# Kernel optimization log

Measured on AMD Instinct MI355X. Metric: run time of the kernel, lower is better.

Reference implementation:

```python
import jax, jax.numpy as jnp
import numpy as np

B, N, DIM = 2, 2048, 1024
H, DH = 8, 64
NUM_BUCKETS, MAX_DISTANCE = 32, 128


def _rel_bucket(rel_pos, num_buckets=NUM_BUCKETS, max_distance=MAX_DISTANCE):
    # torch: n = max(-rel_pos, 0); causal (non-bidirectional) bucketing
    n = jnp.maximum(-rel_pos, 0)
    max_exact = num_buckets // 2
    is_small = n < max_exact
    n_safe = jnp.maximum(n, 1)  # avoid log(0); masked out by is_small anyway
    val_if_large = max_exact + (
        jnp.log(n_safe.astype(jnp.float32) / max_exact)
        / np.log(max_distance / max_exact)
        * (num_buckets - max_exact)
    ).astype(jnp.int32)
    val_if_large = jnp.minimum(val_if_large, num_buckets - 1)
    return jnp.where(is_small, n, val_if_large)


def setup_inputs() -> dict:
    key = jax.random.key(0)
    ks = jax.random.split(key, 10)
    inner = H * DH
    return {
        "x": jax.random.normal(ks[0], (B, N, DIM), jnp.float32),
        "mem_kv": jax.random.normal(ks[1], (B, H * N, 2, DH), jnp.float32),
        "mem_mask": jnp.ones((B, H * N), dtype=bool),
        "Wq": jax.random.normal(ks[2], (DIM, inner), jnp.float32) * (DIM ** -0.5),
        "Wkv": jax.random.normal(ks[3], (DIM, 2 * DH), jnp.float32) * (DIM ** -0.5),
        "Wout": jax.random.normal(ks[4], (inner, DIM), jnp.float32) * (inner ** -0.5),
        "bout": jnp.zeros((DIM,), jnp.float32),
        "rel_emb": jax.random.normal(ks[5], (NUM_BUCKETS, H), jnp.float32),
        "gate": jax.random.normal(ks[6], (H, 1, 1), jnp.float32),
        "null_k": jax.random.normal(ks[7], (DH,), jnp.float32),
        "null_v": jax.random.normal(ks[8], (DH,), jnp.float32),
    }


def reference(x, mem_kv, mem_mask, Wq, Wkv, Wout, bout, rel_emb, gate, null_k, null_v):
    b, n, _ = x.shape
    scale = DH ** -0.5
    q = (x @ Wq).reshape(b, n, H, DH).transpose(0, 2, 1, 3)  # b h n d
    k, v = jnp.split(x @ Wkv, 2, axis=-1)  # each b n d (multi-query: head-shared)

    # local causal attention with T5 relative position bias
    sim = jnp.einsum('bhid,bjd->bhij', q, k) * scale
    pos = jnp.arange(n)
    rel = pos[None, :] - pos[:, None]  # k_pos - q_pos
    bias = rel_emb[_rel_bucket(rel)]  # [n, n, h]
    sim = sim + jnp.transpose(bias, (2, 0, 1))[None] * (DH ** 0.5)
    mask_value = -jnp.finfo(sim.dtype).max
    causal = jnp.triu(jnp.ones((n, n), dtype=bool), 1)
    sim = jnp.where(causal, mask_value, sim)
    attn = jax.nn.softmax(sim, axis=-1)
    local_values = jnp.einsum('bhij,bjd->bhid', attn, v)

    # retrieval (kNN memory) attention branch
    mem = mem_kv.reshape(b, H, n, 2, DH)
    mem_k, mem_v = mem[..., 0, :], mem[..., 1, :]  # b h n d
    null_k_b = jnp.broadcast_to(null_k, (b, H, 1, DH))
    null_v_b = jnp.broadcast_to(null_v, (b, H, 1, DH))
    mem_k = jnp.concatenate([null_k_b, mem_k], axis=2)  # b h (n+1) d
    mem_v = jnp.concatenate([null_v_b, mem_v], axis=2)
    mm = mem_mask.reshape(b, H, 1, n)
    mm = jnp.pad(mm, ((0, 0), (0, 0), (0, 0), (1, 0)), constant_values=True)
    sim_mem = jnp.einsum('bhid,bhjd->bhij', q, mem_k) * scale
    sim_mem = jnp.where(mm, sim_mem, mask_value)
    attn_mem = jax.nn.softmax(sim_mem, axis=-1)
    mem_values = jnp.einsum('bhij,bhjd->bhid', attn_mem, mem_v)

    g = jax.nn.sigmoid(gate)  # [h,1,1] broadcasts over b h n d
    out = local_values * g + mem_values * (1.0 - g)
    out = out.transpose(0, 2, 1, 3).reshape(b, n, H * DH)
    return out @ Wout + bout
```

## Files before the change

kernel.cpp:

```cpp
#include <hip/hip_runtime.h>
#include <hip/hip_fp16.h>

typedef _Float16 f16x8 __attribute__((ext_vector_type(8)));
typedef _Float16 f16x4 __attribute__((ext_vector_type(4)));
typedef __fp16 fp16x2_t __attribute__((ext_vector_type(2)));
typedef float f32x4 __attribute__((ext_vector_type(4)));
typedef float f32x16 __attribute__((ext_vector_type(16)));
typedef unsigned int uint;
typedef uint u32x4 __attribute__((ext_vector_type(4)));

#define NB 2
#define NN 2048
#define NDIM 1024
#define NH 8
#define NDH 64
#define NINNER 512
#define NJM 2080

#define QSCALE 0.18033688011112042f
#define BSCALE 11.541560327111707f


__global__ void conv_x_kernel(const float* __restrict__ x, _Float16* __restrict__ xh) {
  int i = (blockIdx.x * blockDim.x + threadIdx.x) * 4;
  float4 f = *(const float4*)(x + i);
  xh[i + 0] = (_Float16)f.x;
  xh[i + 1] = (_Float16)f.y;
  xh[i + 2] = (_Float16)f.z;
  xh[i + 3] = (_Float16)f.w;
}

__global__ void conv_wt_kernel(const float* __restrict__ Wq, const float* __restrict__ Wkv,
                               _Float16* __restrict__ wt) {
  int idx = blockIdx.x * blockDim.x + threadIdx.x;
  int c = idx >> 10, k = idx & 1023;
  float v = (c < NINNER) ? Wq[(size_t)k * NINNER + c] : Wkv[(size_t)k * 128 + (c - NINNER)];
  wt[idx] = (_Float16)v;
}

__global__ void conv_woutT_kernel(const float* __restrict__ Wout, _Float16* __restrict__ woutT) {
  int idx = blockIdx.x * blockDim.x + threadIdx.x;
  int c = idx >> 9, k = idx & 511;
  woutT[idx] = (_Float16)Wout[(size_t)k * NDIM + c];
}

__global__ __launch_bounds__(256)
void conv_mem_kernel(const float* __restrict__ mem_kv,
                     _Float16* __restrict__ memk, _Float16* __restrict__ memvt) {
  __shared__ _Float16 tv[32][76];
  int jc = blockIdx.x, bh = blockIdx.y;
  int t = threadIdx.x;
  int jl = t >> 3, c = (t & 7) * 8;
  int j0 = jc * 32;
  const float* src = mem_kv + (((size_t)bh * NN) + (j0 + jl)) * 128;
  float4 k0 = *(const float4*)(src + c);
  float4 k1 = *(const float4*)(src + c + 4);
  float4 v0 = *(const float4*)(src + 64 + c);
  float4 v1 = *(const float4*)(src + 64 + c + 4);
  f16x8 kk;
  kk[0]=(_Float16)k0.x; kk[1]=(_Float16)k0.y; kk[2]=(_Float16)k0.z; kk[3]=(_Float16)k0.w;
  kk[4]=(_Float16)k1.x; kk[5]=(_Float16)k1.y; kk[6]=(_Float16)k1.z; kk[7]=(_Float16)k1.w;
  *(f16x8*)(memk + ((size_t)bh * NJM + j0 + jl) * NDH + c) = kk;
  tv[jl][c+0]=(_Float16)v0.x; tv[jl][c+1]=(_Float16)v0.y;
  tv[jl][c+2]=(_Float16)v0.z; tv[jl][c+3]=(_Float16)v0.w;
  tv[jl][c+4]=(_Float16)v1.x; tv[jl][c+5]=(_Float16)v1.y;
  tv[jl][c+6]=(_Float16)v1.z; tv[jl][c+7]=(_Float16)v1.w;
  __syncthreads();
  int d = t >> 2, j8 = (t & 3) * 8;
  f16x8 vv;
#pragma unroll
  for (int u = 0; u < 8; ++u) vv[u] = tv[j8 + u][d];
  *(f16x8*)(memvt + (((size_t)bh * NDH) + d) * NJM + j0 + j8) = vv;
}

__global__ void conv_tail_kernel(const float* __restrict__ null_k, const float* __restrict__ null_v,
                                 _Float16* __restrict__ memk, _Float16* __restrict__ memvt) {
  int t = blockIdx.x * blockDim.x + threadIdx.x;
  int d = t & 63, bh = t >> 6;
  memk[((size_t)bh * NJM + NN) * NDH + d] = (_Float16)null_k[d];
  memvt[(((size_t)bh * NDH) + d) * NJM + NN] = (_Float16)null_v[d];
  for (int r = NN + 1; r < NJM; ++r) {
    memk[((size_t)bh * NJM + r) * NDH + d] = (_Float16)0.f;
    memvt[(((size_t)bh * NDH) + d) * NJM + r] = (_Float16)0.f;
  }
}

__global__ void bias_kernel(const float* __restrict__ rel_emb, float* __restrict__ bias_tab) {
  int idx = blockIdx.x * blockDim.x + threadIdx.x;
  int h = idx >> 11, d = idx & (NN - 1);
  int bucket;
  if (d < 16) bucket = d;
  else {
    float t = logf((float)d * (1.0f / 16.0f)) / 2.0794415416798357f * 16.0f;
    bucket = 16 + (int)t;
    if (bucket > 31) bucket = 31;
  }
  bias_tab[idx] = rel_emb[bucket * NH + h] * BSCALE;
}

__global__ __launch_bounds__(256)
void proj_kernel(const _Float16* __restrict__ xh, const _Float16* __restrict__ wt,
                 _Float16* __restrict__ qh, _Float16* __restrict__ kh, _Float16* __restrict__ vtL) {
  int lane = threadIdx.x & 63, w = threadIdx.x >> 6;
  int wm = w >> 1, wn = w & 1;
  int m0 = blockIdx.x * 64 + wm * 32;
  int n0 = blockIdx.y * 64 + wn * 32;
  int lane_c = lane & 15, lane_g = lane >> 4;
  f32x4 acc[2][2] = {};
  for (int kk = 0; kk < NDIM; kk += 32) {
    f16x8 a[2], bb[2];
#pragma unroll
    for (int s = 0; s < 2; ++s) {
      a[s]  = *(const f16x8*)(xh + (size_t)(m0 + s * 16 + lane_c) * NDIM + kk + lane_g * 8);
      bb[s] = *(const f16x8*)(wt + (size_t)(n0 + s * 16 + lane_c) * NDIM + kk + lane_g * 8);
    }
#pragma unroll
    for (int ms = 0; ms < 2; ++ms)
#pragma unroll
      for (int ns = 0; ns < 2; ++ns)
        acc[ms][ns] = __builtin_amdgcn_mfma_f32_16x16x32_f16(a[ms], bb[ns], acc[ms][ns], 0, 0, 0);
  }
#pragma unroll
  for (int ms = 0; ms < 2; ++ms)
#pragma unroll
    for (int ns = 0; ns < 2; ++ns) {
      int c = n0 + ns * 16 + lane_c;
      int mb = m0 + ms * 16 + lane_g * 4;
      int b = mb >> 11, n = mb & (NN - 1);
      if (c < NINNER) {
        int h = c >> 6, d = c & 63;
#pragma unroll
        for (int r = 0; r < 4; ++r)
          qh[(((size_t)(b * NH + h)) * NN + n + r) * NDH + d] = (_Float16)(acc[ms][ns][r] * QSCALE);
      } else if (c < NINNER + NDH) {
#pragma unroll
        for (int r = 0; r < 4; ++r)
          kh[((size_t)(b * NN + n + r)) * NDH + (c - NINNER)] = (_Float16)acc[ms][ns][r];
      } else {
        f16x4 pv;
#pragma unroll
        for (int r = 0; r < 4; ++r) pv[r] = (_Float16)acc[ms][ns][r];
        *(f16x4*)(vtL + ((size_t)(b * NDH + (c - NINNER - NDH))) * NN + n) = pv;
      }
    }
}


__device__ __forceinline__ uint pkrtz(float a, float b) {
  fp16x2_t t = __builtin_amdgcn_cvt_pkrtz(a, b);
  return __builtin_bit_cast(uint, t);
}

struct K4 { f16x8 k[4]; };

__device__ __forceinline__ K4 load_k4(const _Float16* kp) {
  K4 r;
  r.k[0] = *(const f16x8*)(kp);
  r.k[1] = *(const f16x8*)(kp + 16);
  r.k[2] = *(const f16x8*)(kp + 32);
  r.k[3] = *(const f16x8*)(kp + 48);
  return r;
}

template<int MODE, int LDV>
__device__ __forceinline__ void compute_tile(
    const K4& kc, const _Float16* vp, const f16x8* qf,
    int dd_base, int li, bool hib,
    const float* s_bias, float bias31,
    f32x16& o0, f32x16& o1, float& m, float& l)
{
  f16x8 v00 = *(const f16x8*)(vp);
  f16x8 v01 = *(const f16x8*)(vp + 16);
  f16x8 v10 = *(const f16x8*)(vp + (size_t)32 * LDV);
  f16x8 v11 = *(const f16x8*)(vp + (size_t)32 * LDV + 16);
  f32x16 sA = {}, sB = {};
  sA = __builtin_amdgcn_mfma_f32_32x32x16_f16(kc.k[0], qf[0], sA, 0, 0, 0);
  sB = __builtin_amdgcn_mfma_f32_32x32x16_f16(kc.k[1], qf[1], sB, 0, 0, 0);
  sA = __builtin_amdgcn_mfma_f32_32x32x16_f16(kc.k[2], qf[2], sA, 0, 0, 0);
  sB = __builtin_amdgcn_mfma_f32_32x32x16_f16(kc.k[3], qf[3], sB, 0, 0, 0);
  int hi4 = hib ? 4 : 0;
  float p[16];
  float pmax = -1e30f;
#pragma unroll
  for (int r = 0; r < 16; ++r) {
    int jp = (r & 3) + 8 * (r >> 2) + hi4;
    float v = sA[r] + sB[r];
    if (MODE == 0) { v += bias31; }
    else if (MODE == 1) { int d = dd_base + li - jp; v += (d >= 113) ? bias31 : s_bias[d]; }
    else if (MODE == 2) { int d = li - jp; float bb = s_bias[d < 0 ? 0 : d];
                          v = (jp > li) ? -1e30f : (v + bb); }
    else if (MODE == 4) { v = (jp >= 1) ? -1e30f : v; }
    p[r] = v;
    pmax = fmaxf(pmax, v);
  }
  pmax = fmaxf(pmax, __shfl_xor(pmax, 32));
  if (!__all(pmax <= m + 8.0f)) {
    float mn = fmaxf(m, pmax);
    float f = exp2f(m - mn);
#pragma unroll
    for (int r = 0; r < 16; ++r) { o0[r] *= f; o1[r] *= f; }
    l *= f; m = mn;
  }
  float rs = 0.f;
  uint u[8];
#pragma unroll
  for (int q = 0; q < 8; ++q) {
    float pa = exp2f(p[2 * q] - m), pb = exp2f(p[2 * q + 1] - m);
    rs += pa + pb;
    u[q] = pkrtz(pa, pb);
  }
  rs += __shfl_xor(rs, 32);
  l += rs;
  uint x0 = __shfl_xor(u[0], 32), x1 = __shfl_xor(u[1], 32);
  uint x2 = __shfl_xor(u[2], 32), x3 = __shfl_xor(u[3], 32);
  uint x4 = __shfl_xor(u[4], 32), x5 = __shfl_xor(u[5], 32);
  uint x6 = __shfl_xor(u[6], 32), x7 = __shfl_xor(u[7], 32);
  u32x4 b0u = { hib ? x2 : u[0], hib ? x3 : u[1], hib ? u[2] : x0, hib ? u[3] : x1 };
  u32x4 b1u = { hib ? x6 : u[4], hib ? x7 : u[5], hib ? u[6] : x4, hib ? u[7] : x5 };
  f16x8 b0 = __builtin_bit_cast(f16x8, b0u);
  f16x8 b1 = __builtin_bit_cast(f16x8, b1u);
  o0 = __builtin_amdgcn_mfma_f32_32x32x16_f16(v00, b0, o0, 0, 0, 0);
  o0 = __builtin_amdgcn_mfma_f32_32x32x16_f16(v01, b1, o0, 0, 0, 0);
  o1 = __builtin_amdgcn_mfma_f32_32x32x16_f16(v10, b0, o1, 0, 0, 0);
  o1 = __builtin_amdgcn_mfma_f32_32x32x16_f16(v11, b1, o1, 0, 0, 0);
}

__global__ __launch_bounds__(128, 2)
void attn_kernel(const _Float16* __restrict__ qh, const _Float16* __restrict__ kh,
                 const _Float16* __restrict__ vtL, const _Float16* __restrict__ memk,
                 const _Float16* __restrict__ memvt, const float* __restrict__ bias_tab,
                 const float* __restrict__ gate, _Float16* __restrict__ comb) {
  __shared__ float s_bias[128];
  __shared__ float s_o[2][16][64];
  int bid = blockIdx.x;
  int h = bid & 7, b = (bid >> 3) & 1, qt = 63 - (bid >> 4);
  int tid = threadIdx.x;
  int w = tid >> 6, lane = tid & 63;
  int li = lane & 31;
  bool hib = lane >= 32;
  int i0 = qt * 32;
  int bh = b * NH + h;

  const _Float16* qp = qh + (((size_t)bh * NN) + i0 + li) * NDH + (hib ? 8 : 0);
  f16x8 qf[4];
#pragma unroll
  for (int ks = 0; ks < 4; ++ks) qf[ks] = *(const f16x8*)(qp + ks * 16);

  float gv = gate[h];
  gv = 1.0f / (1.0f + __expf(-gv));
  f32x16 o0 = {}, o1 = {};
  float m = -INFINITY, l = 0.f;

  if (w == 0) {
    s_bias[lane] = bias_tab[h * NN + lane];
    s_bias[lane + 64] = bias_tab[h * NN + lane + 64];
    float bias31 = bias_tab[h * NN + 127];
    const _Float16* kB = kh + (size_t)b * NN * NDH + (size_t)li * NDH + (hib ? 8 : 0);
    const _Float16* vB = vtL + (size_t)b * NDH * NN + (size_t)li * NN + (hib ? 8 : 0);
    int nfar = (i0 - 160) < 0 ? 0 : (((i0 - 160) >> 5) + 1);
    K4 kc = load_k4(kB);
    int t = 0;
    for (; t < nfar; ++t) {
      K4 kn = load_k4(kB + (size_t)(t + 1) * 32 * NDH);
      compute_tile<0, NN>(kc, vB + t * 32, qf, 0, li, hib, s_bias, bias31, o0, o1, m, l);
      kc = kn;
    }
    for (; t < qt; ++t) {
      K4 kn = load_k4(kB + (size_t)(t + 1) * 32 * NDH);
      compute_tile<1, NN>(kc, vB + t * 32, qf, i0 - t * 32, li, hib, s_bias, bias31, o0, o1, m, l);
      kc = kn;
    }
    compute_tile<2, NN>(kc, vB + qt * 32, qf, 0, li, hib, s_bias, bias31, o0, o1, m, l);
  } else {
    const _Float16* kB = memk + (size_t)bh * NJM * NDH + (size_t)li * NDH + (hib ? 8 : 0);
    const _Float16* vB = memvt + (size_t)bh * NDH * NJM + (size_t)li * NJM + (hib ? 8 : 0);
    K4 kc = load_k4(kB);
    for (int t = 0; t < 64; ++t) {
      K4 kn = load_k4(kB + (size_t)(t + 1) * 32 * NDH);
      compute_tile<3, NJM>(kc, vB + t * 32, qf, 0, li, hib, nullptr, 0.f, o0, o1, m, l);
      kc = kn;
    }
    compute_tile<4, NJM>(kc, vB + 64 * 32, qf, 0, li, hib, nullptr, 0.f, o0, o1, m, l);
    float invl = (1.0f - gv) / l;
#pragma unroll
    for (int r = 0; r < 16; ++r) {
      s_o[0][r][lane] = o0[r] * invl;
      s_o[1][r][lane] = o1[r] * invl;
    }
  }
  __syncthreads();
  if (w == 0) {
    float invl = gv / l;
    int i = i0 + li;
    _Float16* cp = comb + ((size_t)(b * NN + i)) * NINNER + h * NDH + (hib ? 4 : 0);
#pragma unroll
    for (int db = 0; db < 2; ++db) {
#pragma unroll
      for (int g = 0; g < 4; ++g) {
        f16x4 st;
#pragma unroll
        for (int r = 0; r < 4; ++r) {
          float ov = (db ? o1[g * 4 + r] : o0[g * 4 + r]) * invl + s_o[db][g * 4 + r][lane];
          st[r] = (_Float16)ov;
        }
        *(f16x4*)(cp + db * 32 + g * 8) = st;
      }
    }
  }
}

__global__ __launch_bounds__(256)
void out_kernel(const _Float16* __restrict__ comb, const _Float16* __restrict__ woutT,
                const float* __restrict__ bout, float* __restrict__ out) {
  int lane = threadIdx.x & 63, w = threadIdx.x >> 6;
  int wm = w >> 1, wn = w & 1;
  int m0 = blockIdx.x * 64 + wm * 32;
  int n0 = blockIdx.y * 64 + wn * 32;
  int lane_c = lane & 15, lane_g = lane >> 4;
  f32x4 acc[2][2] = {};
  for (int kk = 0; kk < NINNER; kk += 32) {
    f16x8 a[2], bb[2];
#pragma unroll
    for (int s = 0; s < 2; ++s) {
      a[s]  = *(const f16x8*)(comb + (size_t)(m0 + s * 16 + lane_c) * NINNER + kk + lane_g * 8);
      bb[s] = *(const f16x8*)(woutT + (size_t)(n0 + s * 16 + lane_c) * NINNER + kk + lane_g * 8);
    }
#pragma unroll
    for (int ms = 0; ms < 2; ++ms)
#pragma unroll
      for (int ns = 0; ns < 2; ++ns)
        acc[ms][ns] = __builtin_amdgcn_mfma_f32_16x16x32_f16(a[ms], bb[ns], acc[ms][ns], 0, 0, 0);
  }
#pragma unroll
  for (int ms = 0; ms < 2; ++ms)
#pragma unroll
    for (int ns = 0; ns < 2; ++ns)
#pragma unroll
      for (int r = 0; r < 4; ++r) {
        int mrow = m0 + ms * 16 + lane_g * 4 + r;
        int c = n0 + ns * 16 + lane_c;
        out[(size_t)mrow * NDIM + c] = acc[ms][ns][r] + bout[c];
      }
}

extern "C" void kernel_launch(void* const* d_in, const int* in_sizes, int n_in,
                              void* d_out, int out_size, void* d_ws, size_t ws_size,
                              hipStream_t stream) {
  const float* x      = (const float*)d_in[0];
  const float* mem_kv = (const float*)d_in[1];
  const float* Wq     = (const float*)d_in[3];
  const float* Wkv    = (const float*)d_in[4];
  const float* Wout   = (const float*)d_in[5];
  const float* bout   = (const float*)d_in[6];
  const float* rel_emb = (const float*)d_in[7];
  const float* gate   = (const float*)d_in[8];
  const float* null_k = (const float*)d_in[9];
  const float* null_v = (const float*)d_in[10];
  float* out = (float*)d_out;
  char* ws = (char*)d_ws;

  _Float16* xh    = (_Float16*)(ws + 0);
  _Float16* wt    = (_Float16*)(ws + 8388608);
  _Float16* woutT = (_Float16*)(ws + 9699328);
  _Float16* qh    = (_Float16*)(ws + 10747904);
  _Float16* kh    = (_Float16*)(ws + 14942208);
  _Float16* vtL   = (_Float16*)(ws + 15466496);
  _Float16* memk  = (_Float16*)(ws + 15990784);
  _Float16* memvt = (_Float16*)(ws + 20250624);
  _Float16* comb  = (_Float16*)(ws + 24510464);
  float* bias_tab = (float*)(ws + 28704768);

  conv_x_kernel<<<4096, 256, 0, stream>>>(x, xh);
  conv_wt_kernel<<<2560, 256, 0, stream>>>(Wq, Wkv, wt);
  conv_woutT_kernel<<<2048, 256, 0, stream>>>(Wout, woutT);
  conv_mem_kernel<<<dim3(64, 16), 256, 0, stream>>>(mem_kv, memk, memvt);
  conv_tail_kernel<<<4, 256, 0, stream>>>(null_k, null_v, memk, memvt);
  bias_kernel<<<64, 256, 0, stream>>>(rel_emb, bias_tab);
  proj_kernel<<<dim3(64, 10), 256, 0, stream>>>(xh, wt, qh, kh, vtL);
  attn_kernel<<<1024, 128, 0, stream>>>(qh, kh, vtL, memk, memvt, bias_tab, gate, comb);
  out_kernel<<<dim3(64, 16), 256, 0, stream>>>(comb, woutT, bout, out);
}
```

Before: 188.9 us.

## Split attention KV range across waves with merge, fuse prep kernels, add setprio

The attention kernel now uses 4 waves instead of 2. Two waves split the local causal tiles by even/odd index and two split the memory tiles in halves, and partial softmax states are merged through shared memory. The small conversion, bias and tail kernels are fused into one prep kernel to cut launch overhead. The K/V row stride is padded to KROWS so prefetch past the end stays in bounds. The change also adds s_setprio around MFMAs and tree reductions for max/sum. Risks are more shared memory and sync per block, plus extra merge arithmetic.

```diff
diff --git a/kernel.cpp b/kernel.cpp
--- a/kernel.cpp
+++ b/kernel.cpp
@@ -16,32 +16,55 @@
 #define NDH 64
 #define NINNER 512
 #define NJM 2080
+#define KROWS 2112
 
 #define QSCALE 0.18033688011112042f
 #define BSCALE 11.541560327111707f
 
-
-__global__ void conv_x_kernel(const float* __restrict__ x, _Float16* __restrict__ xh) {
-  int i = (blockIdx.x * blockDim.x + threadIdx.x) * 4;
-  float4 f = *(const float4*)(x + i);
-  xh[i + 0] = (_Float16)f.x;
-  xh[i + 1] = (_Float16)f.y;
-  xh[i + 2] = (_Float16)f.z;
-  xh[i + 3] = (_Float16)f.w;
-}
-
-__global__ void conv_wt_kernel(const float* __restrict__ Wq, const float* __restrict__ Wkv,
-                               _Float16* __restrict__ wt) {
-  int idx = blockIdx.x * blockDim.x + threadIdx.x;
-  int c = idx >> 10, k = idx & 1023;
-  float v = (c < NINNER) ? Wq[(size_t)k * NINNER + c] : Wkv[(size_t)k * 128 + (c - NINNER)];
-  wt[idx] = (_Float16)v;
-}
-
-__global__ void conv_woutT_kernel(const float* __restrict__ Wout, _Float16* __restrict__ woutT) {
-  int idx = blockIdx.x * blockDim.x + threadIdx.x;
-  int c = idx >> 9, k = idx & 511;
-  woutT[idx] = (_Float16)Wout[(size_t)k * NDIM + c];
+__global__ __launch_bounds__(256)
+void prep_kernel(const float* __restrict__ x, _Float16* __restrict__ xh,
+                 const float* __restrict__ Wq, const float* __restrict__ Wkv,
+                 _Float16* __restrict__ wt,
+                 const float* __restrict__ Wout, _Float16* __restrict__ woutT,
+                 const float* __restrict__ null_k, const float* __restrict__ null_v,
+                 _Float16* __restrict__ memk, _Float16* __restrict__ memvt,
+                 const float* __restrict__ rel_emb, float* __restrict__ bias_tab) {
+  int bx = blockIdx.x, t = threadIdx.x;
+  if (bx < 4096) {
+    int i = (bx * 256 + t) * 4;
+    float4 f = *(const float4*)(x + i);
+    f16x4 o; o[0]=(_Float16)f.x; o[1]=(_Float16)f.y; o[2]=(_Float16)f.z; o[3]=(_Float16)f.w;
+    *(f16x4*)(xh + i) = o;
+  } else if (bx < 6656) {
+    int idx = (bx - 4096) * 256 + t;
+    int c = idx >> 10, k = idx & 1023;
+    float v = (c < NINNER) ? Wq[(size_t)k * NINNER + c] : Wkv[(size_t)k * 128 + (c - NINNER)];
+    wt[idx] = (_Float16)v;
+  } else if (bx < 8704) {
+    int idx = (bx - 6656) * 256 + t;
+    int c = idx >> 9, k = idx & 511;
+    woutT[idx] = (_Float16)Wout[(size_t)k * NDIM + c];
+  } else if (bx < 8768) {
+    int idx = (bx - 8704) * 256 + t;
+    int h = idx >> 11, d = idx & (NN - 1);
+    int bucket;
+    if (d < 16) bucket = d;
+    else {
+      float tt = logf((float)d * (1.0f / 16.0f)) / 2.0794415416798357f * 16.0f;
+      bucket = 16 + (int)tt;
+      if (bucket > 31) bucket = 31;
+    }
+    bias_tab[idx] = rel_emb[bucket * NH + h] * BSCALE;
+  } else {
+    int idx = (bx - 8768) * 256 + t;
+    int d = idx & 63, bh = idx >> 6;
+    memk[((size_t)bh * NJM + NN) * NDH + d] = (_Float16)null_k[d];
+    memvt[(((size_t)bh * NDH) + d) * NJM + NN] = (_Float16)null_v[d];
+    for (int r = NN + 1; r < NJM; ++r) {
+      memk[((size_t)bh * NJM + r) * NDH + d] = (_Float16)0.f;
+      memvt[(((size_t)bh * NDH) + d) * NJM + r] = (_Float16)0.f;
+    }
+  }
 }
 
 __global__ __launch_bounds__(256)
@@ -73,31 +96,6 @@
   *(f16x8*)(memvt + (((size_t)bh * NDH) + d) * NJM + j0 + j8) = vv;
 }
 
-__global__ void conv_tail_kernel(const float* __restrict__ null_k, const float* __restrict__ null_v,
-                                 _Float16* __restrict__ memk, _Float16* __restrict__ memvt) {
-  int t = blockIdx.x * blockDim.x + threadIdx.x;
-  int d = t & 63, bh = t >> 6;
-  memk[((size_t)bh * NJM + NN) * NDH + d] = (_Float16)null_k[d];
-  memvt[(((size_t)bh * NDH) + d) * NJM + NN] = (_Float16)null_v[d];
-  for (int r = NN + 1; r < NJM; ++r) {
-    memk[((size_t)bh * NJM + r) * NDH + d] = (_Float16)0.f;
-    memvt[(((size_t)bh * NDH) + d) * NJM + r] = (_Float16)0.f;
-  }
-}
-
-__global__ void bias_kernel(const float* __restrict__ rel_emb, float* __restrict__ bias_tab) {
-  int idx = blockIdx.x * blockDim.x + threadIdx.x;
-  int h = idx >> 11, d = idx & (NN - 1);
-  int bucket;
-  if (d < 16) bucket = d;
-  else {
-    float t = logf((float)d * (1.0f / 16.0f)) / 2.0794415416798357f * 16.0f;
-    bucket = 16 + (int)t;
-    if (bucket > 31) bucket = 31;
-  }
-  bias_tab[idx] = rel_emb[bucket * NH + h] * BSCALE;
-}
-
 __global__ __launch_bounds__(256)
 void proj_kernel(const _Float16* __restrict__ xh, const _Float16* __restrict__ wt,
                  _Float16* __restrict__ qh, _Float16* __restrict__ kh, _Float16* __restrict__ vtL) {
@@ -135,12 +133,12 @@
       } else if (c < NINNER + NDH) {
 #pragma unroll
         for (int r = 0; r < 4; ++r)
-          kh[((size_t)(b * NN + n + r)) * NDH + (c - NINNER)] = (_Float16)acc[ms][ns][r];
+          kh[((size_t)(b * KROWS + n + r)) * NDH + (c - NINNER)] = (_Float16)acc[ms][ns][r];
       } else {
         f16x4 pv;
 #pragma unroll
         for (int r = 0; r < 4; ++r) pv[r] = (_Float16)acc[ms][ns][r];
-        *(f16x4*)(vtL + ((size_t)(b * NDH + (c - NINNER - NDH))) * NN + n) = pv;
+        *(f16x4*)(vtL + ((size_t)(b * NDH + (c - NINNER - NDH))) * KROWS + n) = pv;
       }
     }
 }
@@ -174,13 +172,14 @@
   f16x8 v10 = *(const f16x8*)(vp + (size_t)32 * LDV);
   f16x8 v11 = *(const f16x8*)(vp + (size_t)32 * LDV + 16);
   f32x16 sA = {}, sB = {};
+  __builtin_amdgcn_s_setprio(1);
   sA = __builtin_amdgcn_mfma_f32_32x32x16_f16(kc.k[0], qf[0], sA, 0, 0, 0);
   sB = __builtin_amdgcn_mfma_f32_32x32x16_f16(kc.k[1], qf[1], sB, 0, 0, 0);
   sA = __builtin_amdgcn_mfma_f32_32x32x16_f16(kc.k[2], qf[2], sA, 0, 0, 0);
   sB = __builtin_amdgcn_mfma_f32_32x32x16_f16(kc.k[3], qf[3], sB, 0, 0, 0);
+  __builtin_amdgcn_s_setprio(0);
   int hi4 = hib ? 4 : 0;
   float p[16];
-  float pmax = -1e30f;
 #pragma unroll
   for (int r = 0; r < 16; ++r) {
     int jp = (r & 3) + 8 * (r >> 2) + hi4;
@@ -191,8 +190,13 @@
                           v = (jp > li) ? -1e30f : (v + bb); }
     else if (MODE == 4) { v = (jp >= 1) ? -1e30f : v; }
     p[r] = v;
-    pmax = fmaxf(pmax, v);
-  }
+  }
+  float t8[8], t4[4];
+#pragma unroll
+  for (int i = 0; i < 8; ++i) t8[i] = fmaxf(p[2 * i], p[2 * i + 1]);
+#pragma unroll
+  for (int i = 0; i < 4; ++i) t4[i] = fmaxf(t8[2 * i], t8[2 * i + 1]);
+  float pmax = fmaxf(fmaxf(t4[0], t4[1]), fmaxf(t4[2], t4[3]));
   pmax = fmaxf(pmax, __shfl_xor(pmax, 32));
   if (!__all(pmax <= m + 8.0f)) {
     float mn = fmaxf(m, pmax);
@@ -201,37 +205,43 @@
     for (int r = 0; r < 16; ++r) { o0[r] *= f; o1[r] *= f; }
     l *= f; m = mn;
   }
-  float rs = 0.f;
-  uint u[8];
-#pragma unroll
-  for (int q = 0; q < 8; ++q) {
-    float pa = exp2f(p[2 * q] - m), pb = exp2f(p[2 * q + 1] - m);
-    rs += pa + pb;
-    u[q] = pkrtz(pa, pb);
-  }
+#pragma unroll
+  for (int r = 0; r < 16; ++r) p[r] = exp2f(p[r] - m);
+#pragma unroll
+  for (int i = 0; i < 8; ++i) t8[i] = p[2 * i] + p[2 * i + 1];
+#pragma unroll
+  for (int i = 0; i < 4; ++i) t4[i] = t8[2 * i] + t8[2 * i + 1];
+  float rs = (t4[0] + t4[1]) + (t4[2] + t4[3]);
   rs += __shfl_xor(rs, 32);
   l += rs;
-  uint x0 = __shfl_xor(u[0], 32), x1 = __shfl_xor(u[1], 32);
-  uint x2 = __shfl_xor(u[2], 32), x3 = __shfl_xor(u[3], 32);
-  uint x4 = __shfl_xor(u[4], 32), x5 = __shfl_xor(u[5], 32);
-  uint x6 = __shfl_xor(u[6], 32), x7 = __shfl_xor(u[7], 32);
-  u32x4 b0u = { hib ? x2 : u[0], hib ? x3 : u[1], hib ? u[2] : x0, hib ? u[3] : x1 };
-  u32x4 b1u = { hib ? x6 : u[4], hib ? x7 : u[5], hib ? u[6] : x4, hib ? u[7] : x5 };
+  uint u0 = pkrtz(p[0], p[1]),   u1 = pkrtz(p[2], p[3]);
+  uint u2 = pkrtz(p[4], p[5]),   u3 = pkrtz(p[6], p[7]);
+  uint u4 = pkrtz(p[8], p[9]),   u5 = pkrtz(p[10], p[11]);
+  uint u6 = pkrtz(p[12], p[13]), u7 = pkrtz(p[14], p[15]);
+  uint x0 = __shfl_xor(u0, 32), x1 = __shfl_xor(u1, 32);
+  uint x2 = __shfl_xor(u2, 32), x3 = __shfl_xor(u3, 32);
+  uint x4 = __shfl_xor(u4, 32), x5 = __shfl_xor(u5, 32);
+  uint x6 = __shfl_xor(u6, 32), x7 = __shfl_xor(u7, 32);
+  u32x4 b0u = { hib ? x2 : u0, hib ? x3 : u1, hib ? u2 : x0, hib ? u3 : x1 };
+  u32x4 b1u = { hib ? x6 : u4, hib ? x7 : u5, hib ? u6 : x4, hib ? u7 : x5 };
   f16x8 b0 = __builtin_bit_cast(f16x8, b0u);
   f16x8 b1 = __builtin_bit_cast(f16x8, b1u);
+  __builtin_amdgcn_s_setprio(1);
   o0 = __builtin_amdgcn_mfma_f32_32x32x16_f16(v00, b0, o0, 0, 0, 0);
   o0 = __builtin_amdgcn_mfma_f32_32x32x16_f16(v01, b1, o0, 0, 0, 0);
   o1 = __builtin_amdgcn_mfma_f32_32x32x16_f16(v10, b0, o1, 0, 0, 0);
   o1 = __builtin_amdgcn_mfma_f32_32x32x16_f16(v11, b1, o1, 0, 0, 0);
-}
-
-__global__ __launch_bounds__(128, 2)
+  __builtin_amdgcn_s_setprio(0);
+}
+
+__global__ __launch_bounds__(256, 4)
 void attn_kernel(const _Float16* __restrict__ qh, const _Float16* __restrict__ kh,
                  const _Float16* __restrict__ vtL, const _Float16* __restrict__ memk,
                  const _Float16* __restrict__ memvt, const float* __restrict__ bias_tab,
                  const float* __restrict__ gate, _Float16* __restrict__ comb) {
-  __shared__ float s_bias[128];
-  __shared__ float s_o[2][16][64];
+  __shared__ float s_bias2[2][128];
+  __shared__ float s_x[2][32][64];
+  __shared__ float s_m[4][32], s_l[4][32];
   int bid = blockIdx.x;
   int h = bid & 7, b = (bid >> 3) & 1, qt = 63 - (bid >> 4);
   int tid = threadIdx.x;
@@ -251,41 +261,71 @@
   f32x16 o0 = {}, o1 = {};
   float m = -INFINITY, l = 0.f;
 
-  if (w == 0) {
+  if (w < 2) {
+    float* s_bias = s_bias2[w];
     s_bias[lane] = bias_tab[h * NN + lane];
     s_bias[lane + 64] = bias_tab[h * NN + lane + 64];
     float bias31 = bias_tab[h * NN + 127];
-    const _Float16* kB = kh + (size_t)b * NN * NDH + (size_t)li * NDH + (hib ? 8 : 0);
-    const _Float16* vB = vtL + (size_t)b * NDH * NN + (size_t)li * NN + (hib ? 8 : 0);
+    const _Float16* kB = kh + (size_t)b * KROWS * NDH + (size_t)li * NDH + (hib ? 8 : 0);
+    const _Float16* vB = vtL + (size_t)b * NDH * KROWS + (size_t)li * KROWS + (hib ? 8 : 0);
     int nfar = (i0 - 160) < 0 ? 0 : (((i0 - 160) >> 5) + 1);
-    K4 kc = load_k4(kB);
-    int t = 0;
-    for (; t < nfar; ++t) {
-      K4 kn = load_k4(kB + (size_t)(t + 1) * 32 * NDH);
-      compute_tile<0, NN>(kc, vB + t * 32, qf, 0, li, hib, s_bias, bias31, o0, o1, m, l);
+    int t = w;
+    K4 kc = load_k4(kB + (size_t)t * 32 * NDH);
+    for (; t < nfar; t += 2) {
+      K4 kn = load_k4(kB + (size_t)(t + 2) * 32 * NDH);
+      compute_tile<0, KROWS>(kc, vB + t * 32, qf, 0, li, hib, s_bias, bias31, o0, o1, m, l);
       kc = kn;
     }
-    for (; t < qt; ++t) {
-      K4 kn = load_k4(kB + (size_t)(t + 1) * 32 * NDH);
-      compute_tile<1, NN>(kc, vB + t * 32, qf, i0 - t * 32, li, hib, s_bias, bias31, o0, o1, m, l);
+    for (; t < qt; t += 2) {
+      K4 kn = load_k4(kB + (size_t)(t + 2) * 32 * NDH);
+      compute_tile<1, KROWS>(kc, vB + t * 32, qf, i0 - t * 32, li, hib, s_bias, bias31, o0, o1, m, l);
       kc = kn;
     }
-    compute_tile<2, NN>(kc, vB + qt * 32, qf, 0, li, hib, s_bias, bias31, o0, o1, m, l);
+    if (t == qt)
+      compute_tile<2, KROWS>(kc, vB + (size_t)qt * 32, qf, 0, li, hib, s_bias, bias31, o0, o1, m, l);
   } else {
     const _Float16* kB = memk + (size_t)bh * NJM * NDH + (size_t)li * NDH + (hib ? 8 : 0);
     const _Float16* vB = memvt + (size_t)bh * NDH * NJM + (size_t)li * NJM + (hib ? 8 : 0);
-    K4 kc = load_k4(kB);
-    for (int t = 0; t < 64; ++t) {
+    int t = (w == 2) ? 0 : 32;
+    int tend = (w == 2) ? 32 : 64;
+    K4 kc = load_k4(kB + (size_t)t * 32 * NDH);
+    for (; t < tend; ++t) {
       K4 kn = load_k4(kB + (size_t)(t + 1) * 32 * NDH);
       compute_tile<3, NJM>(kc, vB + t * 32, qf, 0, li, hib, nullptr, 0.f, o0, o1, m, l);
       kc = kn;
     }
-    compute_tile<4, NJM>(kc, vB + 64 * 32, qf, 0, li, hib, nullptr, 0.f, o0, o1, m, l);
+    if (w == 3)
+      compute_tile<4, NJM>(kc, vB + 64 * 32, qf, 0, li, hib, nullptr, 0.f, o0, o1, m, l);
+  }
+
+  int wpair = w >> 1;
+  if (w & 1) {
+#pragma unroll
+    for (int r = 0; r < 16; ++r) {
+      s_x[wpair][r][lane] = o0[r];
+      s_x[wpair][16 + r][lane] = o1[r];
+    }
+    if (!hib) { s_m[w][li] = m; s_l[w][li] = l; }
+  }
+  __syncthreads();
+  if (!(w & 1)) {
+    float m2 = s_m[w + 1][li], l2 = s_l[w + 1][li];
+    float mm = fmaxf(m, m2);
+    float f1 = exp2f(m - mm), f2 = exp2f(m2 - mm);
+    l = l * f1 + l2 * f2;
+#pragma unroll
+    for (int r = 0; r < 16; ++r) {
+      o0[r] = o0[r] * f1 + s_x[wpair][r][lane] * f2;
+      o1[r] = o1[r] * f1 + s_x[wpair][16 + r][lane] * f2;
+    }
+  }
+  __syncthreads();
+  if (w == 2) {
     float invl = (1.0f - gv) / l;
 #pragma unroll
     for (int r = 0; r < 16; ++r) {
-      s_o[0][r][lane] = o0[r] * invl;
-      s_o[1][r][lane] = o1[r] * invl;
+      s_x[1][r][lane] = o0[r] * invl;
+      s_x[1][16 + r][lane] = o1[r] * invl;
     }
   }
   __syncthreads();
@@ -300,7 +340,7 @@
         f16x4 st;
 #pragma unroll
         for (int r = 0; r < 4; ++r) {
-          float ov = (db ? o1[g * 4 + r] : o0[g * 4 + r]) * invl + s_o[db][g * 4 + r][lane];
+          float ov = (db ? o1[g * 4 + r] : o0[g * 4 + r]) * invl + s_x[1][db * 16 + g * 4 + r][lane];
           st[r] = (_Float16)ov;
         }
         *(f16x4*)(cp + db * 32 + g * 8) = st;
@@ -364,19 +404,16 @@
   _Float16* woutT = (_Float16*)(ws + 9699328);
   _Float16* qh    = (_Float16*)(ws + 10747904);
   _Float16* kh    = (_Float16*)(ws + 14942208);
-  _Float16* vtL   = (_Float16*)(ws + 15466496);
-  _Float16* memk  = (_Float16*)(ws + 15990784);
-  _Float16* memvt = (_Float16*)(ws + 20250624);
-  _Float16* comb  = (_Float16*)(ws + 24510464);
-  float* bias_tab = (float*)(ws + 28704768);
-
-  conv_x_kernel<<<4096, 256, 0, stream>>>(x, xh);
-  conv_wt_kernel<<<2560, 256, 0, stream>>>(Wq, Wkv, wt);
-  conv_woutT_kernel<<<2048, 256, 0, stream>>>(Wout, woutT);
+  _Float16* vtL   = (_Float16*)(ws + 15482880);
+  _Float16* memk  = (_Float16*)(ws + 16023552);
+  _Float16* memvt = (_Float16*)(ws + 20283392);
+  _Float16* comb  = (_Float16*)(ws + 24543232);
+  float* bias_tab = (float*)(ws + 28737536);
+
   conv_mem_kernel<<<dim3(64, 16), 256, 0, stream>>>(mem_kv, memk, memvt);
-  conv_tail_kernel<<<4, 256, 0, stream>>>(null_k, null_v, memk, memvt);
-  bias_kernel<<<64, 256, 0, stream>>>(rel_emb, bias_tab);
+  prep_kernel<<<8772, 256, 0, stream>>>(x, xh, Wq, Wkv, wt, Wout, woutT,
+                                        null_k, null_v, memk, memvt, rel_emb, bias_tab);
   proj_kernel<<<dim3(64, 10), 256, 0, stream>>>(xh, wt, qh, kh, vtL);
-  attn_kernel<<<1024, 128, 0, stream>>>(qh, kh, vtL, memk, memvt, bias_tab, gate, comb);
+  attn_kernel<<<1024, 256, 0, stream>>>(qh, kh, vtL, memk, memvt, bias_tab, gate, comb);
   out_kernel<<<dim3(64, 16), 256, 0, stream>>>(comb, woutT, bout, out);
 }
```

Result: slower. 241.3 us (+27.7%).
